# Kernel tuning notes

Hardware: AMD Instinct MI355X
Metric: run time of the kernel (lower is better)

Reference implementation:

```python
import jax, jax.numpy as jnp
import numpy as np

NUM_HEADS = 12
EPSILON = 1e-6
SCORE_SCALE = 1.0


def setup_inputs() -> dict:
    key = jax.random.key(0)
    ks = jax.random.split(key, 5)
    B, L, E = 2, 2048, 768
    x = jax.random.normal(ks[0], (B, L, E), dtype=jnp.float32)
    attention_mask = jnp.ones((B, L), dtype=jnp.int32)
    # linear params (lecun-ish scale)
    Wqkv = jax.random.normal(ks[1], (E, 3 * E), dtype=jnp.float32) / np.sqrt(E)
    bqkv = jnp.zeros((3 * E,), dtype=jnp.float32)
    Wout = jax.random.normal(ks[2], (E, E), dtype=jnp.float32) / np.sqrt(E)
    bout = jnp.zeros((E,), dtype=jnp.float32)
    return {"x": x, "attention_mask": attention_mask, "Wqkv": Wqkv,
            "bqkv": bqkv, "Wout": Wout, "bout": bout}


def reference(x, attention_mask, Wqkv, bqkv, Wout, bout):
    B, L, E = x.shape
    H = NUM_HEADS
    D = E // H
    qkv = x @ Wqkv + bqkv                      # [B,L,3E]
    q, k, v = jnp.split(qkv, 3, axis=-1)
    q = q.reshape(B, L, H, D).transpose(0, 2, 1, 3)  # [B,H,L,D]
    k = k.reshape(B, L, H, D).transpose(0, 2, 1, 3)
    v = v.reshape(B, L, H, D).transpose(0, 2, 1, 3)

    dot = jnp.einsum('bhid,bhjd->bhij', q, k)        # [B,H,L,L]
    q_sq = jnp.sum(q * q, axis=-1)[..., :, None]     # [B,H,L,1]
    k_sq = jnp.sum(k * k, axis=-1)[..., None, :]     # [B,H,1,L]
    scores = (dot * dot) / (q_sq + k_sq - 2.0 * dot + EPSILON)
    scores = scores * SCORE_SCALE

    pad = attention_mask[:, None, None, :]           # [B,1,1,L]
    scores = jnp.where(pad == 1, scores, jnp.finfo(scores.dtype).min)

    attn = jax.nn.softmax(scores, axis=-1)
    out = jnp.einsum('bhij,bhjd->bhid', attn, v)     # [B,H,L,D]
    out = out.transpose(0, 2, 1, 3).reshape(B, L, E)
    return out @ Wout + bout
```

## Files before the change

kernel.cpp:

```cpp
#include <hip/hip_runtime.h>
#include <hip/hip_bf16.h>
#include <cstdint>
#include <cstddef>


typedef __bf16 bf16_t;
typedef __bf16 bf16x8 __attribute__((ext_vector_type(8)));
typedef __bf16 bf16x4 __attribute__((ext_vector_type(4)));
typedef float floatx4 __attribute__((ext_vector_type(4)));
typedef _Float16 half_t;
typedef _Float16 half4 __attribute__((ext_vector_type(4)));

#define DEVI static __device__ __forceinline__

#define Bc 2
#define Lc 2048
#define Ec 768
#define Hc 12
#define Dc 64
#define N3c 2304
#define Mc 4096
#define ROWSc (Bc * Hc * Lc)

DEVI void glds16(const void* g, void* l) {
  __builtin_amdgcn_global_load_lds(
      (const __attribute__((address_space(1))) void*)g,
      (__attribute__((address_space(3))) void*)l, 16, 0, 0);
}

#define NBCVT 3072
#define NBTC1 1728
#define NBTC2 576

__global__ __launch_bounds__(256) void k_prep(
    const float* __restrict__ x, bf16_t* __restrict__ xb,
    const float* __restrict__ Wqkv, bf16_t* __restrict__ WqT,
    const float* __restrict__ Wout, bf16_t* __restrict__ WoT) {
  const int bid = blockIdx.x, tid = threadIdx.x;
  if (bid < NBCVT) {
    const int i = (bid * 256 + tid) * 4;
    float4 v = *(const float4*)(x + i);
    bf16x4 o;
    o[0] = (bf16_t)v.x; o[1] = (bf16_t)v.y; o[2] = (bf16_t)v.z; o[3] = (bf16_t)v.w;
    *(bf16x4*)(xb + i) = o;
    return;
  }
  __shared__ float tile[32][33];
  const float* in; bf16_t* out; int C, bx, by;
  if (bid < NBCVT + NBTC1) {
    const int r = bid - NBCVT;
    in = Wqkv; out = WqT; C = N3c; bx = r % 72; by = r / 72;
  } else {
    const int r = bid - NBCVT - NBTC1;
    in = Wout; out = WoT; C = Ec; bx = r % 24; by = r / 24;
  }
  const int R = Ec;
  const int c0 = bx * 32, r0 = by * 32;
  const int tx = tid & 31, ty = tid >> 5;
  #pragma unroll
  for (int i = 0; i < 32; i += 8)
    tile[ty + i][tx] = in[(size_t)(r0 + ty + i) * C + c0 + tx];
  __syncthreads();
  #pragma unroll
  for (int i = 0; i < 32; i += 8)
    out[(size_t)(c0 + ty + i) * R + r0 + tx] = (bf16_t)tile[tx][ty + i];
}


DEVI void gemm_core(const bf16_t* __restrict__ A, const bf16_t* __restrict__ Bt,
                    bf16_t* lA, bf16_t* lB, int m0, int n0, floatx4 (&acc)[4][4]) {
  const int tid = threadIdx.x, wave = tid >> 6, lane = tid & 63;
  const int wm = (wave >> 1) * 64, wn = (wave & 1) * 64;
  const int lrow = lane >> 2, lseg = lane & 3;
  const int quad = lane >> 4, r16 = lane & 15;
  for (int kk = 0; kk < 768; kk += 32) {
    glds16(A  + (size_t)(m0 + wave * 32      + lrow) * 768 + kk + lseg * 8, lA + (wave * 32) * 32);
    glds16(A  + (size_t)(m0 + wave * 32 + 16 + lrow) * 768 + kk + lseg * 8, lA + (wave * 32 + 16) * 32);
    glds16(Bt + (size_t)(n0 + wave * 32      + lrow) * 768 + kk + lseg * 8, lB + (wave * 32) * 32);
    glds16(Bt + (size_t)(n0 + wave * 32 + 16 + lrow) * 768 + kk + lseg * 8, lB + (wave * 32 + 16) * 32);
    __syncthreads();
    bf16x8 af[4], bv[4];
    #pragma unroll
    for (int mi = 0; mi < 4; mi++)
      af[mi] = *(const bf16x8*)(lA + (wm + mi * 16 + r16) * 32 + quad * 8);
    #pragma unroll
    for (int ni = 0; ni < 4; ni++)
      bv[ni] = *(const bf16x8*)(lB + (wn + ni * 16 + r16) * 32 + quad * 8);
    #pragma unroll
    for (int mi = 0; mi < 4; mi++)
      #pragma unroll
      for (int ni = 0; ni < 4; ni++)
        acc[mi][ni] = __builtin_amdgcn_mfma_f32_16x16x32_bf16(af[mi], bv[ni], acc[mi][ni], 0, 0, 0);
    __syncthreads();
  }
}

__global__ __launch_bounds__(256) void k_gemm_qkv(
    const bf16_t* __restrict__ A, const bf16_t* __restrict__ Bt,
    const float* __restrict__ bias,
    bf16_t* __restrict__ Qo, bf16_t* __restrict__ Ko, half_t* __restrict__ VTo) {
  __shared__ bf16_t lA[128 * 32];
  __shared__ bf16_t lB[128 * 32];
  const int m0 = blockIdx.y * 128, n0 = blockIdx.x * 128;
  const int tid = threadIdx.x, wave = tid >> 6, lane = tid & 63;
  const int wm = (wave >> 1) * 64, wn = (wave & 1) * 64;
  const int quad = lane >> 4, r16 = lane & 15;
  floatx4 acc[4][4] = {};
  gemm_core(A, Bt, lA, lB, m0, n0, acc);

  const int sec = n0 / 768;
  if (sec == 2) {
    #pragma unroll
    for (int ni = 0; ni < 4; ni++) {
      const int n = n0 + wn + ni * 16 + r16;
      const int nn = n - 1536;
      const int h = nn >> 6, d = nn & 63;
      const float bvs = bias[n];
      #pragma unroll
      for (int mi = 0; mi < 4; mi++) {
        const int m = m0 + wm + mi * 16 + quad * 4;
        const int b = m >> 11, l = m & 2047;
        half4 o;
        #pragma unroll
        for (int reg = 0; reg < 4; reg++) o[reg] = (half_t)(acc[mi][ni][reg] + bvs);
        *(half4*)(VTo + ((size_t)(b * Hc + h) * Dc + d) * Lc + l) = o;
      }
    }
  } else {
    bf16_t* dst = (sec == 0) ? Qo : Ko;
    #pragma unroll
    for (int ni = 0; ni < 4; ni++) {
      const int n = n0 + wn + ni * 16 + r16;
      const int nn = n - sec * 768;
      const int h = nn >> 6, d = nn & 63;
      const float bvs = bias[n];
      #pragma unroll
      for (int mi = 0; mi < 4; mi++) {
        #pragma unroll
        for (int reg = 0; reg < 4; reg++) {
          const int m = m0 + wm + mi * 16 + quad * 4 + reg;
          const int b = m >> 11, l = m & 2047;
          const float v = acc[mi][ni][reg] + bvs;
          dst[(((size_t)(b * Hc + h)) * Lc + l) * Dc + d] = (bf16_t)v;
        }
      }
    }
  }
}

__global__ __launch_bounds__(256) void k_gemm_out(
    const bf16_t* __restrict__ A, const bf16_t* __restrict__ Bt,
    const float* __restrict__ bias, float* __restrict__ out) {
  __shared__ bf16_t lA[128 * 32];
  __shared__ bf16_t lB[128 * 32];
  const int m0 = blockIdx.y * 128, n0 = blockIdx.x * 128;
  const int tid = threadIdx.x, wave = tid >> 6, lane = tid & 63;
  const int wm = (wave >> 1) * 64, wn = (wave & 1) * 64;
  const int quad = lane >> 4, r16 = lane & 15;
  floatx4 acc[4][4] = {};
  gemm_core(A, Bt, lA, lB, m0, n0, acc);
  #pragma unroll
  for (int ni = 0; ni < 4; ni++) {
    const int n = n0 + wn + ni * 16 + r16;
    const float bvs = bias[n];
    #pragma unroll
    for (int mi = 0; mi < 4; mi++) {
      #pragma unroll
      for (int reg = 0; reg < 4; reg++) {
        const int m = m0 + wm + mi * 16 + quad * 4 + reg;
        out[(size_t)m * Ec + n] = acc[mi][ni][reg] + bvs;
      }
    }
  }
}

__global__ __launch_bounds__(256) void k_sq(const bf16_t* __restrict__ Q,
                                            const bf16_t* __restrict__ K,
                                            const int* __restrict__ mask,
                                            float* __restrict__ qsq, float* __restrict__ ksq) {
  const int row = blockIdx.x * 256 + threadIdx.x;
  const bf16x8* q = (const bf16x8*)(Q + (size_t)row * 64);
  const bf16x8* k = (const bf16x8*)(K + (size_t)row * 64);
  float sq = 0.f, sk = 0.f;
  #pragma unroll
  for (int c = 0; c < 8; c++) {
    bf16x8 vq = q[c], vk = k[c];
    #pragma unroll
    for (int j = 0; j < 8; j++) {
      float a = (float)vq[j]; sq += a * a;
      float b = (float)vk[j]; sk += b * b;
    }
  }
  const int bh = row >> 11, l = row & 2047;
  const int b = bh / Hc;
  const int mk = mask[b * Lc + l];
  qsq[row] = sq;
  ksq[row] = (mk == 1) ? (sk + 1e-6f) : -1e30f;
}

__global__ __launch_bounds__(256, 5) void k_attn(
    const bf16_t* __restrict__ Q, const bf16_t* __restrict__ K,
    const half_t* __restrict__ VT, const float* __restrict__ qsq,
    const float* __restrict__ ksq,
    half_t* __restrict__ Op, float* __restrict__ Mp, float* __restrict__ Lp,
    int nS) {
  __shared__ bf16_t lK[2][4096];
  __shared__ half_t lV[2][4096];
  const int gid = blockIdx.x;
  const int s = blockIdx.y;
  const int bh = gid >> 5, qt = gid & 31;
  const int tid = threadIdx.x, wave = tid >> 6, lane = tid & 63;
  const int quad = lane >> 4, r16 = lane & 15;
  const int q0 = qt * 64 + wave * 16;
  const bf16_t* Qh = Q + ((size_t)bh * Lc) * Dc;
  const bf16_t* Kh = K + ((size_t)bh * Lc) * Dc;
  const half_t* VTh = VT + ((size_t)bh * Dc) * Lc;
  const float* qsqh = qsq + bh * Lc;
  const float* ksqh = ksq + bh * Lc;

  const int kt_lo = (32 * s) / nS * 64;
  const int kt_hi = (32 * (s + 1)) / nS * 64;
  const int nt = (kt_hi - kt_lo) >> 6;

  const int p0 = wave * 64 + lane;
  const int srow = p0 >> 3;
  const int sj = (p0 & 7) ^ (srow & 7);
  const bf16_t* kg0 = Kh + (size_t)(kt_lo + srow) * 64 + sj * 8;
  const bf16_t* kg1 = kg0 + 32 * 64;
  const half_t* vg0 = VTh + (size_t)srow * Lc + kt_lo + sj * 8;
  const half_t* vg1 = vg0 + 32 * Lc;
  const int ld0 = wave * 64 * 8, ld1 = (256 + wave * 64) * 8;

  const int sl0 = ((quad ^ (r16 & 7)) * 8);
  const int sl1 = sl0 ^ 32;

  bf16x8 qf0 = *(const bf16x8*)(Qh + (size_t)(q0 + r16) * 64 + quad * 8);
  bf16x8 qf1 = *(const bf16x8*)(Qh + (size_t)(q0 + r16) * 64 + 32 + quad * 8);
  const float qs = qsqh[q0 + r16];
  float mi = -1e30f, li = 0.f;
  floatx4 of[4] = {};

  glds16(kg0, &lK[0][ld0]);
  glds16(kg1, &lK[0][ld1]);
  glds16(vg0, &lV[0][ld0]);
  glds16(vg1, &lV[0][ld1]);
  kg0 += 4096; kg1 += 4096; vg0 += 64; vg1 += 64;
  __syncthreads();

  for (int t = 0; t < nt; t++) {
    const int cur = t & 1;
    if (t + 1 < nt) {
      const int nxt = cur ^ 1;
      glds16(kg0, &lK[nxt][ld0]);
      glds16(kg1, &lK[nxt][ld1]);
      glds16(vg0, &lV[nxt][ld0]);
      glds16(vg1, &lV[nxt][ld1]);
      kg0 += 4096; kg1 += 4096; vg0 += 64; vg1 += 64;
    }
    const int kt = kt_lo + t * 64;
    floatx4 qsk[4];
    #pragma unroll
    for (int c = 0; c < 4; c++)
      qsk[c] = qs + *(const floatx4*)(ksqh + kt + c * 16 + quad * 4);
    floatx4 dot[4];
    #pragma unroll
    for (int c = 0; c < 4; c++) {
      const int rbase = (c * 16 + r16) * 64;
      bf16x8 kf0 = *(const bf16x8*)(&lK[cur][rbase + sl0]);
      bf16x8 kf1 = *(const bf16x8*)(&lK[cur][rbase + sl1]);
      floatx4 a = {};
      a = __builtin_amdgcn_mfma_f32_16x16x32_bf16(kf0, qf0, a, 0, 0, 0);
      a = __builtin_amdgcn_mfma_f32_16x16x32_bf16(kf1, qf1, a, 0, 0, 0);
      dot[c] = a;
    }
    floatx4 sv4[4];
    floatx4 mx = {-1e30f, -1e30f, -1e30f, -1e30f};
    #pragma unroll
    for (int c = 0; c < 4; c++) {
      const floatx4 den = qsk[c] - 2.f * dot[c];
      const floatx4 num = dot[c] * dot[c];
      floatx4 sc;
      #pragma unroll
      for (int e = 0; e < 4; e++) {
        float v = num[e] * __builtin_amdgcn_rcpf(den[e]);
        sc[e] = (qsk[c][e] < 0.f) ? -1e30f : v;
        mx[e] = fmaxf(mx[e], sc[e]);
      }
      sv4[c] = sc;
    }
    float rmax = fmaxf(fmaxf(mx[0], mx[1]), fmaxf(mx[2], mx[3]));
    rmax = fmaxf(rmax, __shfl_xor(rmax, 16));
    rmax = fmaxf(rmax, __shfl_xor(rmax, 32));
    const float mnew = fmaxf(mi, rmax);
    if (__ballot(rmax > mi) != 0ull) {
      const float alpha = __expf(mi - mnew);
      #pragma unroll
      for (int t4 = 0; t4 < 4; t4++) {
        #pragma unroll
        for (int reg = 0; reg < 4; reg++) of[t4][reg] *= alpha;
      }
      li *= alpha;
      mi = mnew;
    }
    half4 pk[4];
    floatx4 ps4 = {};
    #pragma unroll
    for (int c = 0; c < 4; c++) {
      const floatx4 e4 = sv4[c] - mi;
      floatx4 p4;
      #pragma unroll
      for (int e = 0; e < 4; e++) {
        p4[e] = __expf(e4[e]);
        pk[c][e] = (half_t)p4[e];
      }
      ps4 += p4;
    }
    float psum = (ps4[0] + ps4[1]) + (ps4[2] + ps4[3]);
    psum += __shfl_xor(psum, 16);
    psum += __shfl_xor(psum, 32);
    li += psum;
    #pragma unroll
    for (int t4 = 0; t4 < 4; t4++) {
      const int rbase = (t4 * 16 + r16) * 64;
      #pragma unroll
      for (int c = 0; c < 4; c++) {
        const int slot = (2 * c + (quad >> 1)) ^ (r16 & 7);
        half4 va = *(const half4*)(&lV[cur][rbase + slot * 8 + (quad & 1) * 4]);
        of[t4] = __builtin_amdgcn_mfma_f32_16x16x16f16(va, pk[c], of[t4], 0, 0, 0);
      }
    }
    __syncthreads();
  }
  const size_t idx = (size_t)s * ROWSc + (size_t)bh * Lc + q0 + r16;
  #pragma unroll
  for (int t4 = 0; t4 < 4; t4++) {
    half4 o;
    #pragma unroll
    for (int reg = 0; reg < 4; reg++) o[reg] = (half_t)of[t4][reg];
    *(half4*)(Op + idx * 64 + t4 * 16 + quad * 4) = o;
  }
  if (lane < 16) { Mp[idx] = mi; Lp[idx] = li; }
}

__global__ __launch_bounds__(256) void k_merge(
    const half_t* __restrict__ Op, const float* __restrict__ Mp,
    const float* __restrict__ Lp, bf16_t* __restrict__ AO, int nS) {
  const int t = blockIdx.x * 256 + threadIdx.x;
  const int row = t >> 4, dc = (t & 15) * 4;
  float mmax = -1e30f;
  for (int s = 0; s < nS; s++) mmax = fmaxf(mmax, Mp[(size_t)s * ROWSc + row]);
  float L = 0.f;
  float o0 = 0.f, o1 = 0.f, o2 = 0.f, o3 = 0.f;
  for (int s = 0; s < nS; s++) {
    const size_t idx = (size_t)s * ROWSc + row;
    const float w = __expf(Mp[idx] - mmax);
    L += w * Lp[idx];
    const half4 v = *(const half4*)(Op + idx * 64 + dc);
    o0 += w * (float)v[0]; o1 += w * (float)v[1];
    o2 += w * (float)v[2]; o3 += w * (float)v[3];
  }
  const float inv = (L > 0.f) ? __builtin_amdgcn_rcpf(L) : 0.f;
  const int bh = row >> 11, l = row & 2047;
  const int b = bh / Hc, h = bh - b * Hc;
  bf16x4 o;
  o[0] = (bf16_t)(o0 * inv); o[1] = (bf16_t)(o1 * inv);
  o[2] = (bf16_t)(o2 * inv); o[3] = (bf16_t)(o3 * inv);
  *(bf16x4*)(AO + ((size_t)(b * Lc + l)) * Ec + h * 64 + dc) = o;
}


extern "C" void kernel_launch(void* const* d_in, const int* in_sizes, int n_in,
                              void* d_out, int out_size, void* d_ws, size_t ws_size,
                              hipStream_t stream) {
  const float* x    = (const float*)d_in[0];
  const int*   mask = (const int*)d_in[1];
  const float* Wqkv = (const float*)d_in[2];
  const float* bqkv = (const float*)d_in[3];
  const float* Wout = (const float*)d_in[4];
  const float* bout = (const float*)d_in[5];
  float* out = (float*)d_out;

  auto al = [](size_t v) { return (v + 255) & ~(size_t)255; };
  char* ws = (char*)d_ws;
  size_t off = 0;
  auto carve = [&](size_t bytes) -> char* {
    char* p = ws + off;
    off += al(bytes);
    return p;
  };
  bf16_t* WoT = (bf16_t*)carve((size_t)Ec * Ec * 2);
  bf16_t* Qb  = (bf16_t*)carve((size_t)ROWSc * Dc * 2);
  bf16_t* Kb  = (bf16_t*)carve((size_t)ROWSc * Dc * 2);
  half_t* VTb = (half_t*)carve((size_t)ROWSc * Dc * 2);
  bf16_t* AOb = (bf16_t*)carve((size_t)Mc * Ec * 2);
  float*  qsq = (float*)carve((size_t)ROWSc * 4);
  float*  ksq = (float*)carve((size_t)ROWSc * 4);
  const size_t uni = off;
  bf16_t* xb  = (bf16_t*)(ws + uni);
  bf16_t* WqT = (bf16_t*)(ws + uni + al((size_t)Mc * Ec * 2));
  const size_t ph1 = al((size_t)Mc * Ec * 2) + al((size_t)N3c * Ec * 2);
  auto ph2 = [&](int S) {
    return al((size_t)S * ROWSc * Dc * 2) + 2 * al((size_t)S * ROWSc * 4);
  };
  int S = 2;
  for (int cand : {4, 3}) {
    size_t need = uni + (ph1 > ph2(cand) ? ph1 : ph2(cand));
    if (need <= ws_size) { S = cand; break; }
  }
  half_t* Op = (half_t*)(ws + uni);
  float*  Mp = (float*)(ws + uni + al((size_t)S * ROWSc * Dc * 2));
  float*  Lp = (float*)(ws + uni + al((size_t)S * ROWSc * Dc * 2) + al((size_t)S * ROWSc * 4));
  (void)in_sizes; (void)n_in; (void)out_size;

  k_prep<<<NBCVT + NBTC1 + NBTC2, 256, 0, stream>>>(x, xb, Wqkv, WqT, Wout, WoT);
  k_gemm_qkv<<<dim3(N3c / 128, Mc / 128), 256, 0, stream>>>(xb, WqT, bqkv, Qb, Kb, VTb);
  k_sq<<<ROWSc / 256, 256, 0, stream>>>(Qb, Kb, mask, qsq, ksq);
  k_attn<<<dim3(ROWSc / 64, S), 256, 0, stream>>>(Qb, Kb, VTb, qsq, ksq, Op, Mp, Lp, S);
  k_merge<<<ROWSc * 16 / 256, 256, 0, stream>>>(Op, Mp, Lp, AOb, S);
  k_gemm_out<<<dim3(Ec / 128, Mc / 128), 256, 0, stream>>>(AOb, WoT, bout, out);
}
```

Before: 225.4 us.

## Process two 16-row query tiles per wave to reuse K/V LDS fragments

Each wave now handles 32 query rows (two independent 16-row tiles A and B) instead of 16, so every K and V fragment read from LDS feeds two MFMAs. The block covers 128 queries and the grid is halved, which halves K/V global-to-LDS traffic per query. The cost is roughly doubled accumulator and score register state, so the occupancy hint drops from 5 to 4 blocks, and fewer blocks means less parallelism across the device.

```diff
diff --git a/kernel.cpp b/kernel.cpp
--- a/kernel.cpp
+++ b/kernel.cpp
@@ -198,7 +198,7 @@
   ksq[row] = (mk == 1) ? (sk + 1e-6f) : -1e30f;
 }
 
-__global__ __launch_bounds__(256, 5) void k_attn(
+__global__ __launch_bounds__(256, 4) void k_attn(
     const bf16_t* __restrict__ Q, const bf16_t* __restrict__ K,
     const half_t* __restrict__ VT, const float* __restrict__ qsq,
     const float* __restrict__ ksq,
@@ -208,10 +208,10 @@
   __shared__ half_t lV[2][4096];
   const int gid = blockIdx.x;
   const int s = blockIdx.y;
-  const int bh = gid >> 5, qt = gid & 31;
+  const int bh = gid >> 4, qt = gid & 15;
   const int tid = threadIdx.x, wave = tid >> 6, lane = tid & 63;
   const int quad = lane >> 4, r16 = lane & 15;
-  const int q0 = qt * 64 + wave * 16;
+  const int q0 = qt * 128 + wave * 32;
   const bf16_t* Qh = Q + ((size_t)bh * Lc) * Dc;
   const bf16_t* Kh = K + ((size_t)bh * Lc) * Dc;
   const half_t* VTh = VT + ((size_t)bh * Dc) * Lc;
@@ -234,11 +234,14 @@
   const int sl0 = ((quad ^ (r16 & 7)) * 8);
   const int sl1 = sl0 ^ 32;
 
-  bf16x8 qf0 = *(const bf16x8*)(Qh + (size_t)(q0 + r16) * 64 + quad * 8);
-  bf16x8 qf1 = *(const bf16x8*)(Qh + (size_t)(q0 + r16) * 64 + 32 + quad * 8);
-  const float qs = qsqh[q0 + r16];
-  float mi = -1e30f, li = 0.f;
-  floatx4 of[4] = {};
+  bf16x8 qfA0 = *(const bf16x8*)(Qh + (size_t)(q0 + r16) * 64 + quad * 8);
+  bf16x8 qfA1 = *(const bf16x8*)(Qh + (size_t)(q0 + r16) * 64 + 32 + quad * 8);
+  bf16x8 qfB0 = *(const bf16x8*)(Qh + (size_t)(q0 + 16 + r16) * 64 + quad * 8);
+  bf16x8 qfB1 = *(const bf16x8*)(Qh + (size_t)(q0 + 16 + r16) * 64 + 32 + quad * 8);
+  const float qsA = qsqh[q0 + r16];
+  const float qsB = qsqh[q0 + 16 + r16];
+  float miA = -1e30f, liA = 0.f, miB = -1e30f, liB = 0.f;
+  floatx4 ofA[4] = {}, ofB[4] = {};
 
   glds16(kg0, &lK[0][ld0]);
   glds16(kg1, &lK[0][ld1]);
@@ -258,67 +261,95 @@
       kg0 += 4096; kg1 += 4096; vg0 += 64; vg1 += 64;
     }
     const int kt = kt_lo + t * 64;
-    floatx4 qsk[4];
+    floatx4 ks4[4];
     #pragma unroll
     for (int c = 0; c < 4; c++)
-      qsk[c] = qs + *(const floatx4*)(ksqh + kt + c * 16 + quad * 4);
-    floatx4 dot[4];
+      ks4[c] = *(const floatx4*)(ksqh + kt + c * 16 + quad * 4);
+
+    floatx4 dotA[4], dotB[4];
     #pragma unroll
     for (int c = 0; c < 4; c++) {
       const int rbase = (c * 16 + r16) * 64;
       bf16x8 kf0 = *(const bf16x8*)(&lK[cur][rbase + sl0]);
       bf16x8 kf1 = *(const bf16x8*)(&lK[cur][rbase + sl1]);
-      floatx4 a = {};
-      a = __builtin_amdgcn_mfma_f32_16x16x32_bf16(kf0, qf0, a, 0, 0, 0);
-      a = __builtin_amdgcn_mfma_f32_16x16x32_bf16(kf1, qf1, a, 0, 0, 0);
-      dot[c] = a;
-    }
-    floatx4 sv4[4];
-    floatx4 mx = {-1e30f, -1e30f, -1e30f, -1e30f};
+      floatx4 a = {}, bacc = {};
+      a = __builtin_amdgcn_mfma_f32_16x16x32_bf16(kf0, qfA0, a, 0, 0, 0);
+      a = __builtin_amdgcn_mfma_f32_16x16x32_bf16(kf1, qfA1, a, 0, 0, 0);
+      bacc = __builtin_amdgcn_mfma_f32_16x16x32_bf16(kf0, qfB0, bacc, 0, 0, 0);
+      bacc = __builtin_amdgcn_mfma_f32_16x16x32_bf16(kf1, qfB1, bacc, 0, 0, 0);
+      dotA[c] = a;
+      dotB[c] = bacc;
+    }
+
+    floatx4 svA[4], svB[4];
+    floatx4 mxA = {-1e30f, -1e30f, -1e30f, -1e30f};
+    floatx4 mxB = {-1e30f, -1e30f, -1e30f, -1e30f};
     #pragma unroll
     for (int c = 0; c < 4; c++) {
-      const floatx4 den = qsk[c] - 2.f * dot[c];
-      const floatx4 num = dot[c] * dot[c];
-      floatx4 sc;
+      const floatx4 qskA = qsA + ks4[c];
+      const floatx4 qskB = qsB + ks4[c];
+      const floatx4 denA = qskA - 2.f * dotA[c];
+      const floatx4 denB = qskB - 2.f * dotB[c];
+      const floatx4 numA = dotA[c] * dotA[c];
+      const floatx4 numB = dotB[c] * dotB[c];
+      floatx4 scA, scB;
       #pragma unroll
       for (int e = 0; e < 4; e++) {
-        float v = num[e] * __builtin_amdgcn_rcpf(den[e]);
-        sc[e] = (qsk[c][e] < 0.f) ? -1e30f : v;
-        mx[e] = fmaxf(mx[e], sc[e]);
-      }
-      sv4[c] = sc;
-    }
-    float rmax = fmaxf(fmaxf(mx[0], mx[1]), fmaxf(mx[2], mx[3]));
-    rmax = fmaxf(rmax, __shfl_xor(rmax, 16));
-    rmax = fmaxf(rmax, __shfl_xor(rmax, 32));
-    const float mnew = fmaxf(mi, rmax);
-    if (__ballot(rmax > mi) != 0ull) {
-      const float alpha = __expf(mi - mnew);
+        float vA = numA[e] * __builtin_amdgcn_rcpf(denA[e]);
+        float vB = numB[e] * __builtin_amdgcn_rcpf(denB[e]);
+        scA[e] = (qskA[e] < 0.f) ? -1e30f : vA;
+        scB[e] = (qskB[e] < 0.f) ? -1e30f : vB;
+        mxA[e] = fmaxf(mxA[e], scA[e]);
+        mxB[e] = fmaxf(mxB[e], scB[e]);
+      }
+      svA[c] = scA;
+      svB[c] = scB;
+    }
+    float rmaxA = fmaxf(fmaxf(mxA[0], mxA[1]), fmaxf(mxA[2], mxA[3]));
+    float rmaxB = fmaxf(fmaxf(mxB[0], mxB[1]), fmaxf(mxB[2], mxB[3]));
+    rmaxA = fmaxf(rmaxA, __shfl_xor(rmaxA, 16));
+    rmaxB = fmaxf(rmaxB, __shfl_xor(rmaxB, 16));
+    rmaxA = fmaxf(rmaxA, __shfl_xor(rmaxA, 32));
+    rmaxB = fmaxf(rmaxB, __shfl_xor(rmaxB, 32));
+    const float mnewA = fmaxf(miA, rmaxA);
+    const float mnewB = fmaxf(miB, rmaxB);
+    if (__ballot((rmaxA > miA) || (rmaxB > miB)) != 0ull) {
+      const float alphaA = __expf(miA - mnewA);
+      const float alphaB = __expf(miB - mnewB);
       #pragma unroll
       for (int t4 = 0; t4 < 4; t4++) {
         #pragma unroll
-        for (int reg = 0; reg < 4; reg++) of[t4][reg] *= alpha;
-      }
-      li *= alpha;
-      mi = mnew;
-    }
-    half4 pk[4];
-    floatx4 ps4 = {};
+        for (int reg = 0; reg < 4; reg++) {
+          ofA[t4][reg] *= alphaA;
+          ofB[t4][reg] *= alphaB;
+        }
+      }
+      liA *= alphaA; liB *= alphaB;
+      miA = mnewA; miB = mnewB;
+    }
+    half4 pkA[4], pkB[4];
+    floatx4 psA = {}, psB = {};
     #pragma unroll
     for (int c = 0; c < 4; c++) {
-      const floatx4 e4 = sv4[c] - mi;
-      floatx4 p4;
+      const floatx4 eA = svA[c] - miA;
+      const floatx4 eB = svB[c] - miB;
       #pragma unroll
       for (int e = 0; e < 4; e++) {
-        p4[e] = __expf(e4[e]);
-        pk[c][e] = (half_t)p4[e];
-      }
-      ps4 += p4;
-    }
-    float psum = (ps4[0] + ps4[1]) + (ps4[2] + ps4[3]);
-    psum += __shfl_xor(psum, 16);
-    psum += __shfl_xor(psum, 32);
-    li += psum;
+        const float pA = __expf(eA[e]);
+        const float pB = __expf(eB[e]);
+        psA[e] += pA; psB[e] += pB;
+        pkA[c][e] = (half_t)pA;
+        pkB[c][e] = (half_t)pB;
+      }
+    }
+    float psumA = (psA[0] + psA[1]) + (psA[2] + psA[3]);
+    float psumB = (psB[0] + psB[1]) + (psB[2] + psB[3]);
+    psumA += __shfl_xor(psumA, 16);
+    psumB += __shfl_xor(psumB, 16);
+    psumA += __shfl_xor(psumA, 32);
+    psumB += __shfl_xor(psumB, 32);
+    liA += psumA; liB += psumB;
+
     #pragma unroll
     for (int t4 = 0; t4 < 4; t4++) {
       const int rbase = (t4 * 16 + r16) * 64;
@@ -326,20 +357,29 @@
       for (int c = 0; c < 4; c++) {
         const int slot = (2 * c + (quad >> 1)) ^ (r16 & 7);
         half4 va = *(const half4*)(&lV[cur][rbase + slot * 8 + (quad & 1) * 4]);
-        of[t4] = __builtin_amdgcn_mfma_f32_16x16x16f16(va, pk[c], of[t4], 0, 0, 0);
+        ofA[t4] = __builtin_amdgcn_mfma_f32_16x16x16f16(va, pkA[c], ofA[t4], 0, 0, 0);
+        ofB[t4] = __builtin_amdgcn_mfma_f32_16x16x16f16(va, pkB[c], ofB[t4], 0, 0, 0);
       }
     }
     __syncthreads();
   }
-  const size_t idx = (size_t)s * ROWSc + (size_t)bh * Lc + q0 + r16;
+  const size_t idxA = (size_t)s * ROWSc + (size_t)bh * Lc + q0 + r16;
+  const size_t idxB = idxA + 16;
   #pragma unroll
   for (int t4 = 0; t4 < 4; t4++) {
-    half4 o;
-    #pragma unroll
-    for (int reg = 0; reg < 4; reg++) o[reg] = (half_t)of[t4][reg];
-    *(half4*)(Op + idx * 64 + t4 * 16 + quad * 4) = o;
-  }
-  if (lane < 16) { Mp[idx] = mi; Lp[idx] = li; }
+    half4 oA, oB;
+    #pragma unroll
+    for (int reg = 0; reg < 4; reg++) {
+      oA[reg] = (half_t)ofA[t4][reg];
+      oB[reg] = (half_t)ofB[t4][reg];
+    }
+    *(half4*)(Op + idxA * 64 + t4 * 16 + quad * 4) = oA;
+    *(half4*)(Op + idxB * 64 + t4 * 16 + quad * 4) = oB;
+  }
+  if (lane < 16) {
+    Mp[idxA] = miA; Lp[idxA] = liA;
+    Mp[idxB] = miB; Lp[idxB] = liB;
+  }
 }
 
 __global__ __launch_bounds__(256) void k_merge(
@@ -415,7 +455,7 @@
   k_prep<<<NBCVT + NBTC1 + NBTC2, 256, 0, stream>>>(x, xb, Wqkv, WqT, Wout, WoT);
   k_gemm_qkv<<<dim3(N3c / 128, Mc / 128), 256, 0, stream>>>(xb, WqT, bqkv, Qb, Kb, VTb);
   k_sq<<<ROWSc / 256, 256, 0, stream>>>(Qb, Kb, mask, qsq, ksq);
-  k_attn<<<dim3(ROWSc / 64, S), 256, 0, stream>>>(Qb, Kb, VTb, qsq, ksq, Op, Mp, Lp, S);
+  k_attn<<<dim3(ROWSc / 128, S), 256, 0, stream>>>(Qb, Kb, VTb, qsq, ksq, Op, Mp, Lp, S);
   k_merge<<<ROWSc * 16 / 256, 256, 0, stream>>>(Op, Mp, Lp, AOb, S);
   k_gemm_out<<<dim3(Ec / 128, Mc / 128), 256, 0, stream>>>(AOb, WoT, bout, out);
 }
```

Result: slower. 258.5 us (+14.7%).
